# Kernel optimization log

Measured on AMD Instinct MI355X. Metric: run time of the kernel, lower is better.

## Reference

```python
import jax, jax.numpy as jnp
import numpy as np

T, H, NH, NKV, HD = 2048, 1024, 16, 4, 64
I, E, TOPK = 2048, 8, 2
EPS = 1e-5
ROPE_BASE = 10000.0


def rms_norm(x, w):
    var = jnp.mean(x * x, axis=-1, keepdims=True)
    return x * jax.lax.rsqrt(var + EPS) * w


def apply_rope(x, positions, n_heads):
    # neox-style rotary over full head_dim
    t = x.reshape(-1, n_heads, HD)
    half = HD // 2
    inv_freq = 1.0 / (ROPE_BASE ** (jnp.arange(0, half, dtype=jnp.float32) / half))
    freqs = positions.astype(jnp.float32)[:, None] * inv_freq[None, :]  # [T, half]
    cos = jnp.cos(freqs)[:, None, :]
    sin = jnp.sin(freqs)[:, None, :]
    x1, x2 = t[..., :half], t[..., half:]
    rot = jnp.concatenate([x1 * cos - x2 * sin, x2 * cos + x1 * sin], axis=-1)
    return rot.reshape(x.shape)


def setup_inputs():
    key = jax.random.key(0)
    ks = jax.random.split(key, 9)
    s = 0.02
    return dict(
        positions=jnp.arange(T, dtype=jnp.int32),
        hidden_states=jax.random.normal(ks[0], (T, H), jnp.float32),
        input_ln_w=jnp.ones((H,), jnp.float32),
        post_ln_w=jnp.ones((H,), jnp.float32),
        residual_ln_w=jnp.ones((H,), jnp.float32),
        qkv_w=jax.random.normal(ks[1], ((NH + 2 * NKV) * HD, H), jnp.float32) * s,
        o_w=jax.random.normal(ks[2], (H, NH * HD), jnp.float32) * s,
        gate_w=jax.random.normal(ks[3], (E, H), jnp.float32) * s,
        ws=jax.random.normal(ks[4], (E, 2 * I, H), jnp.float32) * s,
        w2s=jax.random.normal(ks[5], (E, H, I), jnp.float32) * s,
        res_w13=jax.random.normal(ks[6], (2 * H, H), jnp.float32) * s,
        res_w2=jax.random.normal(ks[7], (H, H), jnp.float32) * s,
    )


def attention(x, positions, qkv_w, o_w):
    qkv = x @ qkv_w.T  # [T, (NH+2*NKV)*HD]
    q, k, v = jnp.split(qkv, [NH * HD, NH * HD + NKV * HD], axis=-1)
    q = apply_rope(q, positions, NH)
    k = apply_rope(k, positions, NKV)
    q = q.reshape(T, NH, HD)
    k = k.reshape(T, NKV, HD)
    v = v.reshape(T, NKV, HD)
    rep = NH // NKV  # GQA: repeat kv heads
    k = jnp.repeat(k, rep, axis=1)
    v = jnp.repeat(v, rep, axis=1)
    scale = HD ** -0.5
    scores = jnp.einsum('tnd,snd->nts', q, k) * scale  # [NH, T, T]
    causal = jnp.tril(jnp.ones((T, T), dtype=bool))
    scores = jnp.where(causal[None], scores, -jnp.inf)
    probs = jax.nn.softmax(scores, axis=-1)
    out = jnp.einsum('nts,snd->tnd', probs, v).reshape(T, NH * HD)
    return out @ o_w.T


def silu_and_mul(gu):
    g, u = jnp.split(gu, 2, axis=-1)
    return jax.nn.silu(g) * u


def moe(x, gate_w, ws, w2s):
    logits = x @ gate_w.T  # [T, E]
    probs = jax.nn.softmax(logits, axis=-1)
    topk_w, topk_ids = jax.lax.top_k(probs, TOPK)
    topk_w = topk_w / jnp.sum(topk_w, axis=-1, keepdims=True)  # renormalize (top_k > 1)
    routes = jnp.zeros((x.shape[0], E), x.dtype).at[
        jnp.arange(x.shape[0])[:, None], topk_ids].set(topk_w)  # [T, E] sparse routing
    gu = jnp.einsum('th,eih->tei', x, ws)        # [T, E, 2I]
    act = silu_and_mul(gu)                        # [T, E, I]
    eo = jnp.einsum('tei,ehi->teh', act, w2s)     # [T, E, H]
    return jnp.einsum('te,teh->th', routes, eo)


def reference(positions, hidden_states, input_ln_w, post_ln_w, residual_ln_w,
              qkv_w, o_w, gate_w, ws, w2s, res_w13, res_w2):
    residual_input = hidden_states
    h = rms_norm(hidden_states, input_ln_w)
    h = attention(h, positions, qkv_w, o_w)
    residual_attn = residual_input + h
    # parallel residual MLP branch (ffn_dim == hidden)
    r = rms_norm(residual_attn, residual_ln_w)
    r = silu_and_mul(r @ res_w13.T) @ res_w2.T
    residual_mlp = residual_attn + r
    # MoE branch
    m = rms_norm(residual_attn, post_ln_w)
    m = moe(m, gate_w, ws, w2s)
    return residual_mlp + m
```

## Files before the change

kernel.cpp:

```cpp
#include <hip/hip_runtime.h>
#include <stdint.h>


typedef _Float16 f16;
typedef _Float16 f16x8 __attribute__((ext_vector_type(8)));
typedef _Float16 f16x4 __attribute__((ext_vector_type(4)));
typedef float f32x4 __attribute__((ext_vector_type(4)));

#define DEV __device__ __forceinline__

DEV void glds16(const void* g, void* l) {
  __builtin_amdgcn_global_load_lds((const __attribute__((address_space(1))) void*)g,
                                   (__attribute__((address_space(3))) void*)l, 16, 0, 0);
}

__global__ void cvt_f16_kernel(const float* __restrict__ in, f16* __restrict__ outp) {
  const size_t i = ((size_t)blockIdx.x * 256 + threadIdx.x) * 4;
  float4 f = *(const float4*)(in + i);
  f16x4 o;
  o[0] = (f16)f.x; o[1] = (f16)f.y; o[2] = (f16)f.z; o[3] = (f16)f.w;
  *(f16x4*)(outp + i) = o;
}

__global__ void cvt_f16x2_kernel(const float* __restrict__ in,
                                 f16* __restrict__ oh, f16* __restrict__ ol) {
  const size_t i = ((size_t)blockIdx.x * 256 + threadIdx.x) * 4;
  float4 f = *(const float4*)(in + i);
  f16x4 h, l;
  h[0] = (f16)f.x; l[0] = (f16)(f.x - (float)h[0]);
  h[1] = (f16)f.y; l[1] = (f16)(f.y - (float)h[1]);
  h[2] = (f16)f.z; l[2] = (f16)(f.z - (float)h[2]);
  h[3] = (f16)f.w; l[3] = (f16)(f.w - (float)h[3]);
  *(f16x4*)(oh + i) = h;
  *(f16x4*)(ol + i) = l;
}

__global__ void rmsnorm_kernel(const float* __restrict__ in, const float* __restrict__ w,
                               f16* __restrict__ outp) {
  const int t = blockIdx.x * 4 + (threadIdx.x >> 6);
  const int lane = threadIdx.x & 63;
  const float* x = in + (size_t)t * 1024;
  float v[16]; float ss = 0.f;
#pragma unroll
  for (int j = 0; j < 16; j++) { float a = x[lane + 64 * j]; v[j] = a; ss += a * a; }
#pragma unroll
  for (int m = 1; m < 64; m <<= 1) ss += __shfl_xor(ss, m);
  const float rs = rsqrtf(ss * (1.f / 1024.f) + 1e-5f);
#pragma unroll
  for (int j = 0; j < 16; j++)
    outp[(size_t)t * 1024 + lane + 64 * j] = (f16)(v[j] * rs * w[lane + 64 * j]);
}

__global__ void rmsnorm_dual_kernel(const float* __restrict__ in,
                                    const float* __restrict__ w1, const float* __restrict__ w2,
                                    f16* __restrict__ o1, f16* __restrict__ o2) {
  const int t = blockIdx.x * 4 + (threadIdx.x >> 6);
  const int lane = threadIdx.x & 63;
  const float* x = in + (size_t)t * 1024;
  float v[16]; float ss = 0.f;
#pragma unroll
  for (int j = 0; j < 16; j++) { float a = x[lane + 64 * j]; v[j] = a; ss += a * a; }
#pragma unroll
  for (int m = 1; m < 64; m <<= 1) ss += __shfl_xor(ss, m);
  const float rs = rsqrtf(ss * (1.f / 1024.f) + 1e-5f);
#pragma unroll
  for (int j = 0; j < 16; j++) {
    float nv = v[j] * rs;
    size_t idx = (size_t)t * 1024 + lane + 64 * j;
    o1[idx] = (f16)(nv * w1[lane + 64 * j]);
    o2[idx] = (f16)(nv * w2[lane + 64 * j]);
  }
}

template <int EPI, int BN>
__global__ __launch_bounds__(256) void gemm_f16_kernel(
    const f16* __restrict__ A, const f16* __restrict__ B,
    void* __restrict__ outp, const float* __restrict__ addsrc,
    int M, int N, int K) {
  constexpr int JT = BN / 32;
  __shared__ __attribute__((aligned(16))) f16 As[2][128 * 32];
  __shared__ __attribute__((aligned(16))) f16 Bs[2][BN * 32];
  const int tid = threadIdx.x;
  const size_t row0 = (size_t)blockIdx.y * 128, col0 = (size_t)blockIdx.x * BN;
  const int c0 = tid, c1 = tid + 256;
  const f16* a0 = A + (row0 + (c0 >> 2)) * K + (c0 & 3) * 8;
  const f16* a1 = A + (row0 + (c1 >> 2)) * K + (c1 & 3) * 8;
  const f16* b0 = B + (col0 + (c0 >> 2)) * K + (c0 & 3) * 8;
  const f16* b1 = B + (col0 + ((BN == 128) ? (c1 >> 2) : 0)) * K + (c1 & 3) * 8;

  const int wave = tid >> 6, lane = tid & 63, lr = lane >> 4, lc = lane & 15;
  const int wr = wave >> 1, wc = wave & 1;

  f32x4 acc[4][JT];
#pragma unroll
  for (int i = 0; i < 4; i++)
#pragma unroll
    for (int j = 0; j < JT; j++) acc[i][j] = (f32x4){0.f, 0.f, 0.f, 0.f};

  auto stage = [&](int k0, int buf) {
    glds16(a0 + k0, As[buf] + c0 * 8);
    glds16(a1 + k0, As[buf] + c1 * 8);
    glds16(b0 + k0, Bs[buf] + c0 * 8);
    if constexpr (BN == 128) glds16(b1 + k0, Bs[buf] + c1 * 8);
  };

  stage(0, 0);
  __syncthreads();
  int cur = 0;
  for (int k0 = 0; k0 < K; k0 += 32) {
    if (k0 + 32 < K) stage(k0 + 32, cur ^ 1);
    f16x8 af[4], bfr[JT];
#pragma unroll
    for (int i = 0; i < 4; i++)
      af[i] = *(const f16x8*)(As[cur] + (wr * 64 + i * 16 + lc) * 32 + lr * 8);
#pragma unroll
    for (int j = 0; j < JT; j++)
      bfr[j] = *(const f16x8*)(Bs[cur] + (wc * (BN / 2) + j * 16 + lc) * 32 + lr * 8);
#pragma unroll
    for (int i = 0; i < 4; i++)
#pragma unroll
      for (int j = 0; j < JT; j++)
        acc[i][j] = __builtin_amdgcn_mfma_f32_16x16x32_f16(af[i], bfr[j], acc[i][j], 0, 0, 0);
    __syncthreads();
    cur ^= 1;
  }

#pragma unroll
  for (int i = 0; i < 4; i++)
#pragma unroll
    for (int j = 0; j < JT; j++) {
      const size_t rbase = row0 + wr * 64 + i * 16 + lr * 4;
      const size_t col = col0 + wc * (BN / 2) + j * 16 + lc;
#pragma unroll
      for (int r = 0; r < 4; r++) {
        size_t idx = (rbase + r) * N + col;
        if constexpr (EPI == 0) ((float*)outp)[idx] = acc[i][j][r];
        else if constexpr (EPI == 1) ((float*)outp)[idx] = acc[i][j][r] + addsrc[idx];
        else ((f16*)outp)[idx] = (f16)acc[i][j][r];
      }
    }
}

__global__ __launch_bounds__(256) void gemm_f16x2_add_kernel(
    const f16* __restrict__ Ah, const f16* __restrict__ Al,
    const f16* __restrict__ Bh, const f16* __restrict__ Bl,
    float* __restrict__ outp, const float* __restrict__ addsrc,
    int M, int N, int K) {
  __shared__ __attribute__((aligned(16))) f16 Ash[2][128 * 32];
  __shared__ __attribute__((aligned(16))) f16 Asl[2][128 * 32];
  __shared__ __attribute__((aligned(16))) f16 Bsh[2][64 * 32];
  __shared__ __attribute__((aligned(16))) f16 Bsl[2][64 * 32];
  const int tid = threadIdx.x;
  const size_t row0 = (size_t)blockIdx.y * 128, col0 = (size_t)blockIdx.x * 64;
  const int c0 = tid, c1 = tid + 256;
  const size_t aoff0 = (row0 + (c0 >> 2)) * K + (c0 & 3) * 8;
  const size_t aoff1 = (row0 + (c1 >> 2)) * K + (c1 & 3) * 8;
  const size_t boff0 = (col0 + (c0 >> 2)) * K + (c0 & 3) * 8;

  const int wave = tid >> 6, lane = tid & 63, lr = lane >> 4, lc = lane & 15;
  const int wr = wave >> 1, wc = wave & 1;

  f32x4 acc[4][2];
#pragma unroll
  for (int i = 0; i < 4; i++)
#pragma unroll
    for (int j = 0; j < 2; j++) acc[i][j] = (f32x4){0.f, 0.f, 0.f, 0.f};

  auto stage = [&](int k0, int buf) {
    glds16(Ah + aoff0 + k0, Ash[buf] + c0 * 8);
    glds16(Ah + aoff1 + k0, Ash[buf] + c1 * 8);
    glds16(Al + aoff0 + k0, Asl[buf] + c0 * 8);
    glds16(Al + aoff1 + k0, Asl[buf] + c1 * 8);
    glds16(Bh + boff0 + k0, Bsh[buf] + c0 * 8);
    glds16(Bl + boff0 + k0, Bsl[buf] + c0 * 8);
  };

  stage(0, 0);
  __syncthreads();
  int cur = 0;
  for (int k0 = 0; k0 < K; k0 += 32) {
    if (k0 + 32 < K) stage(k0 + 32, cur ^ 1);
    f16x8 afh[4], afl[4], bfh[2], bfl[2];
#pragma unroll
    for (int i = 0; i < 4; i++) {
      const int ro = (wr * 64 + i * 16 + lc) * 32 + lr * 8;
      afh[i] = *(const f16x8*)(Ash[cur] + ro);
      afl[i] = *(const f16x8*)(Asl[cur] + ro);
    }
#pragma unroll
    for (int j = 0; j < 2; j++) {
      const int ro = (wc * 32 + j * 16 + lc) * 32 + lr * 8;
      bfh[j] = *(const f16x8*)(Bsh[cur] + ro);
      bfl[j] = *(const f16x8*)(Bsl[cur] + ro);
    }
#pragma unroll
    for (int i = 0; i < 4; i++)
#pragma unroll
      for (int j = 0; j < 2; j++) {
        acc[i][j] = __builtin_amdgcn_mfma_f32_16x16x32_f16(afh[i], bfh[j], acc[i][j], 0, 0, 0);
        acc[i][j] = __builtin_amdgcn_mfma_f32_16x16x32_f16(afh[i], bfl[j], acc[i][j], 0, 0, 0);
        acc[i][j] = __builtin_amdgcn_mfma_f32_16x16x32_f16(afl[i], bfh[j], acc[i][j], 0, 0, 0);
      }
    __syncthreads();
    cur ^= 1;
  }

#pragma unroll
  for (int i = 0; i < 4; i++)
#pragma unroll
    for (int j = 0; j < 2; j++) {
      const size_t rbase = row0 + wr * 64 + i * 16 + lr * 4;
      const size_t col = col0 + wc * 32 + j * 16 + lc;
#pragma unroll
      for (int r = 0; r < 4; r++) {
        size_t idx = (rbase + r) * N + col;
        outp[idx] = acc[i][j][r] + addsrc[idx];
      }
    }
}

template <int DIVROW, int BN>
__global__ __launch_bounds__(256) void gemm_moe_kernel(
    const f16* __restrict__ A, const f16* __restrict__ Ball, f16* __restrict__ outp,
    const int* __restrict__ perm, const int* __restrict__ counts,
    int N, int K, size_t strideB) {
  constexpr int JT = BN / 32;
  const int e = blockIdx.z;
  const int cnt = counts[e];
  const int bm = blockIdx.y;
  if (bm * 128 >= cnt) return;
  const f16* B = Ball + (size_t)e * strideB;
  __shared__ __attribute__((aligned(16))) f16 As[2][128 * 32];
  __shared__ __attribute__((aligned(16))) f16 Bs[2][BN * 32];
  const int tid = threadIdx.x;
  const size_t col0 = (size_t)blockIdx.x * BN;
  const int c0 = tid, c1 = tid + 256;
  const int pbase = e * 2048 + bm * 128;
  const int rt0 = c0 >> 2, rt1 = c1 >> 2;
  const int sid0 = (bm * 128 + rt0 < cnt) ? perm[pbase + rt0] : -1;
  const int sid1 = (bm * 128 + rt1 < cnt) ? perm[pbase + rt1] : -1;
  const size_t ar0 = DIVROW ? (size_t)(sid0 >> 1) : (size_t)sid0;
  const size_t ar1 = DIVROW ? (size_t)(sid1 >> 1) : (size_t)sid1;
  const f16* ap0 = A + ar0 * K + (c0 & 3) * 8;
  const f16* ap1 = A + ar1 * K + (c1 & 3) * 8;
  const f16* b0 = B + (col0 + (c0 >> 2)) * K + (c0 & 3) * 8;
  const f16* b1 = B + (col0 + ((BN == 128) ? (c1 >> 2) : 0)) * K + (c1 & 3) * 8;

  const int wave = tid >> 6, lane = tid & 63, lr = lane >> 4, lc = lane & 15;
  const int wr = wave >> 1, wc = wave & 1;

  f32x4 acc[4][JT];
#pragma unroll
  for (int i = 0; i < 4; i++)
#pragma unroll
    for (int j = 0; j < JT; j++) acc[i][j] = (f32x4){0.f, 0.f, 0.f, 0.f};

  auto stageB = [&](int k0, int buf) {
    glds16(b0 + k0, Bs[buf] + c0 * 8);
    if constexpr (BN == 128) glds16(b1 + k0, Bs[buf] + c1 * 8);
  };
  auto loadA = [&](int k0, f16x8& va0, f16x8& va1) {
#pragma unroll
    for (int x = 0; x < 8; x++) { va0[x] = (f16)0.f; va1[x] = (f16)0.f; }
    if (sid0 >= 0) va0 = *(const f16x8*)(ap0 + k0);
    if (sid1 >= 0) va1 = *(const f16x8*)(ap1 + k0);
  };

  f16x8 va0, va1;
  loadA(0, va0, va1);
  stageB(0, 0);
  *(f16x8*)(As[0] + c0 * 8) = va0;
  *(f16x8*)(As[0] + c1 * 8) = va1;
  __syncthreads();
  int cur = 0;
  for (int k0 = 0; k0 < K; k0 += 32) {
    const bool nxt = (k0 + 32 < K);
    if (nxt) { stageB(k0 + 32, cur ^ 1); loadA(k0 + 32, va0, va1); }
    f16x8 af[4], bfr[JT];
#pragma unroll
    for (int i = 0; i < 4; i++)
      af[i] = *(const f16x8*)(As[cur] + (wr * 64 + i * 16 + lc) * 32 + lr * 8);
#pragma unroll
    for (int j = 0; j < JT; j++)
      bfr[j] = *(const f16x8*)(Bs[cur] + (wc * (BN / 2) + j * 16 + lc) * 32 + lr * 8);
#pragma unroll
    for (int i = 0; i < 4; i++)
#pragma unroll
      for (int j = 0; j < JT; j++)
        acc[i][j] = __builtin_amdgcn_mfma_f32_16x16x32_f16(af[i], bfr[j], acc[i][j], 0, 0, 0);
    if (nxt) {
      *(f16x8*)(As[cur ^ 1] + c0 * 8) = va0;
      *(f16x8*)(As[cur ^ 1] + c1 * 8) = va1;
    }
    __syncthreads();
    cur ^= 1;
  }

  int sids[4][4];
#pragma unroll
  for (int i = 0; i < 4; i++)
#pragma unroll
    for (int r = 0; r < 4; r++) {
      int rit = wr * 64 + i * 16 + lr * 4 + r;
      sids[i][r] = (bm * 128 + rit < cnt) ? perm[pbase + rit] : -1;
    }
#pragma unroll
  for (int i = 0; i < 4; i++)
#pragma unroll
    for (int j = 0; j < JT; j++) {
      const size_t col = col0 + wc * (BN / 2) + j * 16 + lc;
#pragma unroll
      for (int r = 0; r < 4; r++)
        if (sids[i][r] >= 0)
          outp[(size_t)sids[i][r] * N + col] = (f16)acc[i][j][r];
    }
}

__global__ void rope_kernel(const float* __restrict__ qkv, const int* __restrict__ pos,
                            f16* __restrict__ qr, f16* __restrict__ kr) {
  const int t = blockIdx.y;
  const int u = blockIdx.x * 256 + threadIdx.x;
  if (u >= 640) return;
  const float* base = qkv + (size_t)t * 1536;
  const int head = u >> 5, i = u & 31;
  const bool isq = head < 16;
  const int off = isq ? head * 64 + i : 1024 + (head - 16) * 64 + i;
  const float x1 = base[off], x2 = base[off + 32];
  const double ph = (double)pos[t] * exp((double)i * -0.28782313662425575);
  const float c = (float)cos(ph), s = (float)sin(ph);
  const float r1 = x1 * c - x2 * s, r2 = x2 * c + x1 * s;
  if (isq) {
    const float qs = 0.18033688011116042f;
    qr[(size_t)t * 1024 + head * 64 + i] = (f16)(qs * r1);
    qr[(size_t)t * 1024 + head * 64 + i + 32] = (f16)(qs * r2);
  } else {
    const int kh = head - 16;
    kr[(size_t)t * 256 + kh * 64 + i] = (f16)r1;
    kr[(size_t)t * 256 + kh * 64 + i + 32] = (f16)r2;
  }
}

__global__ void vtrans_kernel(const float* __restrict__ qkvf, f16* __restrict__ vt) {
  __shared__ float Ts[64 * 69];
  const int t0 = blockIdx.x * 64;
  const int kv = blockIdx.y;
  const int tid = threadIdx.x;
  const int tr = tid >> 2, jj = tid & 3;
  const float* src = qkvf + (size_t)(t0 + tr) * 1536 + 1280 + kv * 64 + jj * 16;
#pragma unroll
  for (int x = 0; x < 4; x++) {
    float4 f = *(const float4*)(src + x * 4);
    Ts[tr * 69 + jj * 16 + x * 4 + 0] = f.x;
    Ts[tr * 69 + jj * 16 + x * 4 + 1] = f.y;
    Ts[tr * 69 + jj * 16 + x * 4 + 2] = f.z;
    Ts[tr * 69 + jj * 16 + x * 4 + 3] = f.w;
  }
  __syncthreads();
  f16* dst = vt + (size_t)(kv * 64 + tr) * 2048 + t0 + jj * 16;
#pragma unroll
  for (int x = 0; x < 2; x++) {
    f16x8 o;
#pragma unroll
    for (int i = 0; i < 8; i++) o[i] = (f16)Ts[(jj * 16 + x * 8 + i) * 69 + tr];
    *(f16x8*)(dst + x * 8) = o;
  }
}

__global__ __launch_bounds__(256, 3) void attn_kernel(
    const f16* __restrict__ qr, const f16* __restrict__ kr, const f16* __restrict__ vt,
    f16* __restrict__ ahi, f16* __restrict__ alo) {
  const int qt = 31 - (int)blockIdx.x;
  const int h = blockIdx.y;
  const int kvh = h >> 2;
  __shared__ __attribute__((aligned(16))) f16 Ks[128 * 72];
  __shared__ __attribute__((aligned(16))) f16 Vs[64 * 136];
  __shared__ __attribute__((aligned(16))) f16 Pl[4 * 16 * 136];
  const int tid = threadIdx.x;
  const int wave = tid >> 6, lane = tid & 63, lr = lane >> 4, lc = lane & 15;
  const int trow = qt * 64 + wave * 16 + lc;
  f16* Pw = Pl + wave * 16 * 136;

  const int krow = tid >> 3, kcol = (tid & 7) * 8;
  const int vrow = tid >> 4, vcol = (tid & 15) * 8;
  const f16* kgbase = kr + (size_t)kvh * 64 + kcol;
  const f16* vgbase = vt + (size_t)(kvh * 64 + vrow) * 2048 + vcol;

  const f16* qp = qr + (size_t)trow * 1024 + h * 64 + lr * 8;
  f16x8 qf0 = *(const f16x8*)(qp);
  f16x8 qf1 = *(const f16x8*)(qp + 32);

  float m_run = -3e38f, l_run = 0.f;
  f32x4 accO[4];
#pragma unroll
  for (int jo = 0; jo < 4; jo++) accO[jo] = (f32x4){0.f, 0.f, 0.f, 0.f};

  const int nch = (qt >> 1) + 1;

  f16x8 kreg[4], vreg[4];
#pragma unroll
  for (int it = 0; it < 4; it++) {
    kreg[it] = *(const f16x8*)(kgbase + (size_t)(it * 32 + krow) * 256);
    vreg[it] = *(const f16x8*)(vgbase + it * 16 * 2048);
  }

  for (int ch = 0; ch < nch; ++ch) {
    const int c0 = ch * 128;
    const bool last = (ch == nch - 1);

    __syncthreads();
#pragma unroll
    for (int it = 0; it < 4; it++) {
      *(f16x8*)(Ks + (it * 32 + krow) * 72 + kcol) = kreg[it];
      *(f16x8*)(Vs + (it * 16 + vrow) * 136 + vcol) = vreg[it];
    }
    __syncthreads();

    if (!last) {
      const int c1 = c0 + 128;
#pragma unroll
      for (int it = 0; it < 4; it++) {
        kreg[it] = *(const f16x8*)(kgbase + (size_t)(c1 + it * 32 + krow) * 256);
        vreg[it] = *(const f16x8*)(vgbase + it * 16 * 2048 + c1);
      }
    }

    f32x4 st[8];
#pragma unroll
    for (int j = 0; j < 8; j++) {
      const f16* kp = Ks + (j * 16 + lc) * 72 + lr * 8;
      f16x8 ka0 = *(const f16x8*)(kp);
      f16x8 ka1 = *(const f16x8*)(kp + 32);
      f32x4 s = (f32x4){0.f, 0.f, 0.f, 0.f};
      s = __builtin_amdgcn_mfma_f32_16x16x32_f16(ka0, qf0, s, 0, 0, 0);
      s = __builtin_amdgcn_mfma_f32_16x16x32_f16(ka1, qf1, s, 0, 0, 0);
      st[j] = s;
    }

    if (last) {
#pragma unroll
      for (int j = 0; j < 8; j++)
#pragma unroll
        for (int r = 0; r < 4; r++)
          if (c0 + j * 16 + lr * 4 + r > trow) st[j][r] = -3e38f;
    }

    float mc = -3e38f;
#pragma unroll
    for (int j = 0; j < 8; j++)
      mc = fmaxf(mc, fmaxf(fmaxf(st[j][0], st[j][1]), fmaxf(st[j][2], st[j][3])));
    mc = fmaxf(mc, __shfl_xor(mc, 16));
    mc = fmaxf(mc, __shfl_xor(mc, 32));
    const float mn = fmaxf(m_run, mc);
    const float alpha = __builtin_amdgcn_exp2f(m_run - mn);
    m_run = mn;

    float ls = 0.f;
#pragma unroll
    for (int j = 0; j < 8; j++) {
      f16x4 pv;
#pragma unroll
      for (int r = 0; r < 4; r++) {
        float e = __builtin_amdgcn_exp2f(st[j][r] - mn);
        ls += e;
        pv[r] = (f16)e;
      }
      *(f16x4*)(Pw + lc * 136 + j * 16 + lr * 4) = pv;
    }
    ls += __shfl_xor(ls, 16);
    ls += __shfl_xor(ls, 32);
    l_run = l_run * alpha + ls;
#pragma unroll
    for (int jo = 0; jo < 4; jo++) accO[jo] *= alpha;

#pragma unroll
    for (int kkt = 0; kkt < 4; kkt++) {
      f16x8 pb = *(const f16x8*)(Pw + lc * 136 + kkt * 32 + lr * 8);
#pragma unroll
      for (int jo = 0; jo < 4; jo++) {
        f16x8 va = *(const f16x8*)(Vs + (jo * 16 + lc) * 136 + kkt * 32 + lr * 8);
        accO[jo] = __builtin_amdgcn_mfma_f32_16x16x32_f16(va, pb, accO[jo], 0, 0, 0);
      }
    }
  }

  const float inv = 1.f / l_run;
#pragma unroll
  for (int jo = 0; jo < 4; jo++) {
    f16x4 hi4, lo4;
#pragma unroll
    for (int r = 0; r < 4; r++) {
      float o = accO[jo][r] * inv;
      f16 hv = (f16)o;
      hi4[r] = hv;
      lo4[r] = (f16)(o - (float)hv);
    }
    const size_t idx = (size_t)trow * 1024 + h * 64 + jo * 16 + lr * 4;
    *(f16x4*)(ahi + idx) = hi4;
    *(f16x4*)(alo + idx) = lo4;
  }
}

__global__ void routing_kernel(const float* __restrict__ resA,
                               const float* __restrict__ postw,
                               const float* __restrict__ gw,
                               int* __restrict__ counts, int* __restrict__ perm,
                               float* __restrict__ rw) {
  const int t = blockIdx.x * 4 + (threadIdx.x >> 6);
  const int lane = threadIdx.x & 63;
  const float* x = resA + (size_t)t * 1024;
  float v[16]; float ss = 0.f;
#pragma unroll
  for (int j = 0; j < 16; j++) { float a = x[lane + 64 * j]; v[j] = a; ss += a * a; }
#pragma unroll
  for (int m = 1; m < 64; m <<= 1) ss += __shfl_xor(ss, m);
  const float rs = rsqrtf(ss * (1.f / 1024.f) + 1e-5f);
#pragma unroll
  for (int j = 0; j < 16; j++) v[j] *= rs * postw[lane + 64 * j];
  float lg[8];
#pragma unroll
  for (int e = 0; e < 8; e++) {
    float p = 0.f;
    const float* g = gw + (size_t)e * 1024;
#pragma unroll
    for (int j = 0; j < 16; j++) p += v[j] * g[lane + 64 * j];
#pragma unroll
    for (int m = 1; m < 64; m <<= 1) p += __shfl_xor(p, m);
    lg[e] = p;
  }
  if (lane == 0) {
    int e0 = 0; float b0 = lg[0];
#pragma unroll
    for (int e = 1; e < 8; e++) if (lg[e] > b0) { b0 = lg[e]; e0 = e; }
    int e1 = -1; float b1 = -3e38f;
#pragma unroll
    for (int e = 0; e < 8; e++) if (e != e0 && lg[e] > b1) { b1 = lg[e]; e1 = e; }
    const float w0 = 1.f / (1.f + expf(b1 - b0));
    const float w1 = 1.f - w0;
    int p0 = atomicAdd(&counts[e0], 1);
    perm[e0 * 2048 + p0] = t * 2;
    int p1 = atomicAdd(&counts[e1], 1);
    perm[e1 * 2048 + p1] = t * 2 + 1;
    rw[t * 2] = w0;
    rw[t * 2 + 1] = w1;
  }
}

__global__ void silu_mul_kernel(const f16* __restrict__ gu, f16* __restrict__ outp, int lgN) {
  const int N = 1 << lgN;
  const size_t i4 = ((size_t)blockIdx.x * 256 + threadIdx.x) * 4;
  const size_t r = i4 >> lgN;
  const int c = (int)(i4 & (N - 1));
  const f16* gp = gu + r * (size_t)(2 * N) + c;
  f16x4 g = *(const f16x4*)gp;
  f16x4 u = *(const f16x4*)(gp + N);
  f16x4 o;
#pragma unroll
  for (int x = 0; x < 4; x++) {
    float gg = (float)g[x], uu = (float)u[x];
    o[x] = (f16)(gg / (1.f + __expf(-gg)) * uu);
  }
  *(f16x4*)(outp + r * (size_t)N + c) = o;
}

__global__ void final_add_kernel(float* __restrict__ outp, const f16* __restrict__ eo,
                                 const float* __restrict__ rw) {
  const size_t i4 = ((size_t)blockIdx.x * 256 + threadIdx.x) * 4;
  const int t = (int)(i4 >> 10);
  const int c = (int)(i4 & 1023);
  const float w0 = rw[2 * t], w1 = rw[2 * t + 1];
  f16x4 a = *(const f16x4*)(eo + ((size_t)(2 * t)) * 1024 + c);
  f16x4 b = *(const f16x4*)(eo + ((size_t)(2 * t + 1)) * 1024 + c);
  float4 o = *(float4*)(outp + i4);
  o.x += w0 * (float)a[0] + w1 * (float)b[0];
  o.y += w0 * (float)a[1] + w1 * (float)b[1];
  o.z += w0 * (float)a[2] + w1 * (float)b[2];
  o.w += w0 * (float)a[3] + w1 * (float)b[3];
  *(float4*)(outp + i4) = o;
}

extern "C" void kernel_launch(void* const* d_in, const int* in_sizes, int n_in,
                              void* d_out, int out_size, void* d_ws, size_t ws_size,
                              hipStream_t stream) {
  const int* positions = (const int*)d_in[0];
  const float* hidden = (const float*)d_in[1];
  const float* in_ln = (const float*)d_in[2];
  const float* post_ln = (const float*)d_in[3];
  const float* res_ln = (const float*)d_in[4];
  const float* qkv_w = (const float*)d_in[5];
  const float* o_w = (const float*)d_in[6];
  const float* gate_w = (const float*)d_in[7];
  const float* ws_w = (const float*)d_in[8];
  const float* w2s_w = (const float*)d_in[9];
  const float* w13_w = (const float*)d_in[10];
  const float* w2_w = (const float*)d_in[11];
  float* out = (float*)d_out;

  char* p = (char*)d_ws;
  auto alloc = [&](size_t b) { void* r = (void*)p; p += (b + 255) & ~(size_t)255; return r; };

  f16* wqkv = (f16*)alloc((size_t)1536 * 1024 * 2);
  f16* woh  = (f16*)alloc((size_t)1024 * 1024 * 2);
  f16* wol  = (f16*)alloc((size_t)1024 * 1024 * 2);
  f16* wws  = (f16*)alloc((size_t)8 * 4096 * 1024 * 2);
  f16* ww2  = (f16*)alloc((size_t)8 * 1024 * 2048 * 2);
  f16* w13  = (f16*)alloc((size_t)2048 * 1024 * 2);
  f16* w2c  = (f16*)alloc((size_t)1024 * 1024 * 2);
  f16* hn   = (f16*)alloc((size_t)2048 * 1024 * 2);
  float* qkvf = (float*)alloc((size_t)2048 * 1536 * 4);
  f16* qr = (f16*)alloc((size_t)2048 * 1024 * 2);
  f16* kr = (f16*)alloc((size_t)2048 * 256 * 2);
  f16* vt = (f16*)alloc((size_t)256 * 2048 * 2);
  f16* ath = (f16*)alloc((size_t)2048 * 1024 * 2);
  f16* atl = (f16*)alloc((size_t)2048 * 1024 * 2);
  float* resA = (float*)alloc((size_t)2048 * 1024 * 4);
  f16* rn = (f16*)alloc((size_t)2048 * 1024 * 2);
  f16* mn = (f16*)alloc((size_t)2048 * 1024 * 2);
  f16* gu13 = (f16*)alloc((size_t)2048 * 2048 * 2);
  f16* act13 = (f16*)alloc((size_t)2048 * 1024 * 2);
  f16* gum = (f16*)alloc((size_t)4096 * 4096 * 2);
  f16* actm = (f16*)alloc((size_t)4096 * 2048 * 2);
  f16* eo = (f16*)alloc((size_t)4096 * 1024 * 2);
  float* rw = (float*)alloc((size_t)4096 * 4);
  int* counts = (int*)alloc(256);
  int* perm = (int*)alloc((size_t)8 * 2048 * 4);

  cvt_f16_kernel<<<dim3(1536 * 1024 / 1024), dim3(256), 0, stream>>>(qkv_w, wqkv);
  cvt_f16_kernel<<<dim3(8 * 4096 * 1024 / 1024), dim3(256), 0, stream>>>(ws_w, wws);
  cvt_f16_kernel<<<dim3(8 * 1024 * 2048 / 1024), dim3(256), 0, stream>>>(w2s_w, ww2);
  cvt_f16_kernel<<<dim3(2048 * 1024 / 1024), dim3(256), 0, stream>>>(w13_w, w13);
  cvt_f16_kernel<<<dim3(1024 * 1024 / 1024), dim3(256), 0, stream>>>(w2_w, w2c);
  cvt_f16x2_kernel<<<dim3(1024 * 1024 / 1024), dim3(256), 0, stream>>>(o_w, woh, wol);
  hipMemsetAsync(counts, 0, 256, stream);

  rmsnorm_kernel<<<dim3(512), dim3(256), 0, stream>>>(hidden, in_ln, hn);
  gemm_f16_kernel<0, 64><<<dim3(24, 16), dim3(256), 0, stream>>>(
      hn, wqkv, (void*)qkvf, (const float*)nullptr, 2048, 1536, 1024);
  rope_kernel<<<dim3(3, 2048), dim3(256), 0, stream>>>(qkvf, positions, qr, kr);
  vtrans_kernel<<<dim3(32, 4), dim3(256), 0, stream>>>(qkvf, vt);
  attn_kernel<<<dim3(32, 16), dim3(256), 0, stream>>>(qr, kr, vt, ath, atl);
  gemm_f16x2_add_kernel<<<dim3(16, 16), dim3(256), 0, stream>>>(
      ath, atl, woh, wol, resA, hidden, 2048, 1024, 1024);

  rmsnorm_dual_kernel<<<dim3(512), dim3(256), 0, stream>>>(resA, res_ln, post_ln, rn, mn);
  routing_kernel<<<dim3(512), dim3(256), 0, stream>>>(resA, post_ln, gate_w, counts, perm, rw);

  gemm_f16_kernel<2, 64><<<dim3(32, 16), dim3(256), 0, stream>>>(
      rn, w13, (void*)gu13, (const float*)nullptr, 2048, 2048, 1024);
  silu_mul_kernel<<<dim3(2048 * 1024 / 1024), dim3(256), 0, stream>>>(gu13, act13, 10);
  gemm_f16_kernel<1, 64><<<dim3(16, 16), dim3(256), 0, stream>>>(
      act13, w2c, (void*)out, resA, 2048, 1024, 1024);

  gemm_moe_kernel<1, 128><<<dim3(32, 16, 8), dim3(256), 0, stream>>>(
      mn, wws, gum, perm, counts, 4096, 1024, (size_t)4096 * 1024);
  silu_mul_kernel<<<dim3(4096 * 2048 / 1024), dim3(256), 0, stream>>>(gum, actm, 11);
  gemm_moe_kernel<0, 128><<<dim3(8, 16, 8), dim3(256), 0, stream>>>(
      actm, ww2, eo, perm, counts, 1024, 2048, (size_t)1024 * 2048);
  final_add_kernel<<<dim3(2048 * 1024 / 1024), dim3(256), 0, stream>>>(out, eo, rw);
}
```

Before: 661.1 us.

## Split-K the small GEMMs and MoE down projection, reducing partials in consumers

Adds a split-K template parameter to the dense, f16x2 and MoE GEMM kernels. The QKV, O-proj, residual down-proj and MoE down-proj GEMMs now write fp32 partial results, which are summed by rope/vtrans, a new add3 kernel, or final_add4. The goal is more blocks and better CU occupancy for GEMMs whose grids are small (256 to 384 blocks). The cost is extra fp32 partial-buffer traffic, two extra elementwise launches, and fp32 instead of f16 expert outputs, which is a 4x split for the MoE output.

After: 642.8 us. 1.03x faster.

```diff
diff --git a/kernel.cpp b/kernel.cpp
--- a/kernel.cpp
+++ b/kernel.cpp
@@ -72,7 +72,7 @@
   }
 }
 
-template <int EPI, int BN>
+template <int EPI, int BN, int SPLITK = 1>
 __global__ __launch_bounds__(256) void gemm_f16_kernel(
     const f16* __restrict__ A, const f16* __restrict__ B,
     void* __restrict__ outp, const float* __restrict__ addsrc,
@@ -82,6 +82,8 @@
   __shared__ __attribute__((aligned(16))) f16 Bs[2][BN * 32];
   const int tid = threadIdx.x;
   const size_t row0 = (size_t)blockIdx.y * 128, col0 = (size_t)blockIdx.x * BN;
+  const int ks = (SPLITK > 1) ? (int)blockIdx.z : 0;
+  const int kspan = K / SPLITK, kb = ks * kspan;
   const int c0 = tid, c1 = tid + 256;
   const f16* a0 = A + (row0 + (c0 >> 2)) * K + (c0 & 3) * 8;
   const f16* a1 = A + (row0 + (c1 >> 2)) * K + (c1 & 3) * 8;
@@ -104,11 +106,11 @@
     if constexpr (BN == 128) glds16(b1 + k0, Bs[buf] + c1 * 8);
   };
 
-  stage(0, 0);
+  stage(kb, 0);
   __syncthreads();
   int cur = 0;
-  for (int k0 = 0; k0 < K; k0 += 32) {
-    if (k0 + 32 < K) stage(k0 + 32, cur ^ 1);
+  for (int k0 = kb; k0 < kb + kspan; k0 += 32) {
+    if (k0 + 32 < kb + kspan) stage(k0 + 32, cur ^ 1);
     f16x8 af[4], bfr[JT];
 #pragma unroll
     for (int i = 0; i < 4; i++)
@@ -134,13 +136,16 @@
 #pragma unroll
       for (int r = 0; r < 4; r++) {
         size_t idx = (rbase + r) * N + col;
-        if constexpr (EPI == 0) ((float*)outp)[idx] = acc[i][j][r];
+        if constexpr (SPLITK > 1) {
+          ((float*)outp)[(size_t)ks * M * N + idx] = acc[i][j][r];
+        } else if constexpr (EPI == 0) ((float*)outp)[idx] = acc[i][j][r];
         else if constexpr (EPI == 1) ((float*)outp)[idx] = acc[i][j][r] + addsrc[idx];
         else ((f16*)outp)[idx] = (f16)acc[i][j][r];
       }
     }
 }
 
+template <int SPLITK>
 __global__ __launch_bounds__(256) void gemm_f16x2_add_kernel(
     const f16* __restrict__ Ah, const f16* __restrict__ Al,
     const f16* __restrict__ Bh, const f16* __restrict__ Bl,
@@ -152,6 +157,8 @@
   __shared__ __attribute__((aligned(16))) f16 Bsl[2][64 * 32];
   const int tid = threadIdx.x;
   const size_t row0 = (size_t)blockIdx.y * 128, col0 = (size_t)blockIdx.x * 64;
+  const int ks = (SPLITK > 1) ? (int)blockIdx.z : 0;
+  const int kspan = K / SPLITK, kb = ks * kspan;
   const int c0 = tid, c1 = tid + 256;
   const size_t aoff0 = (row0 + (c0 >> 2)) * K + (c0 & 3) * 8;
   const size_t aoff1 = (row0 + (c1 >> 2)) * K + (c1 & 3) * 8;
@@ -175,11 +182,11 @@
     glds16(Bl + boff0 + k0, Bsl[buf] + c0 * 8);
   };
 
-  stage(0, 0);
+  stage(kb, 0);
   __syncthreads();
   int cur = 0;
-  for (int k0 = 0; k0 < K; k0 += 32) {
-    if (k0 + 32 < K) stage(k0 + 32, cur ^ 1);
+  for (int k0 = kb; k0 < kb + kspan; k0 += 32) {
+    if (k0 + 32 < kb + kspan) stage(k0 + 32, cur ^ 1);
     f16x8 afh[4], afl[4], bfh[2], bfl[2];
 #pragma unroll
     for (int i = 0; i < 4; i++) {
@@ -214,21 +221,24 @@
 #pragma unroll
       for (int r = 0; r < 4; r++) {
         size_t idx = (rbase + r) * N + col;
-        outp[idx] = acc[i][j][r] + addsrc[idx];
+        if constexpr (SPLITK > 1) outp[(size_t)ks * M * N + idx] = acc[i][j][r];
+        else outp[idx] = acc[i][j][r] + addsrc[idx];
       }
     }
 }
 
-template <int DIVROW, int BN>
+template <int DIVROW, int BN, int SPLITK = 1>
 __global__ __launch_bounds__(256) void gemm_moe_kernel(
-    const f16* __restrict__ A, const f16* __restrict__ Ball, f16* __restrict__ outp,
+    const f16* __restrict__ A, const f16* __restrict__ Ball, void* __restrict__ outp,
     const int* __restrict__ perm, const int* __restrict__ counts,
     int N, int K, size_t strideB) {
   constexpr int JT = BN / 32;
-  const int e = blockIdx.z;
+  const int e = (int)blockIdx.z / SPLITK;
+  const int ks = (int)blockIdx.z % SPLITK;
   const int cnt = counts[e];
   const int bm = blockIdx.y;
   if (bm * 128 >= cnt) return;
+  const int kspan = K / SPLITK, kb = ks * kspan;
   const f16* B = Ball + (size_t)e * strideB;
   __shared__ __attribute__((aligned(16))) f16 As[2][128 * 32];
   __shared__ __attribute__((aligned(16))) f16 Bs[2][BN * 32];
@@ -267,14 +277,14 @@
   };
 
   f16x8 va0, va1;
-  loadA(0, va0, va1);
-  stageB(0, 0);
+  loadA(kb, va0, va1);
+  stageB(kb, 0);
   *(f16x8*)(As[0] + c0 * 8) = va0;
   *(f16x8*)(As[0] + c1 * 8) = va1;
   __syncthreads();
   int cur = 0;
-  for (int k0 = 0; k0 < K; k0 += 32) {
-    const bool nxt = (k0 + 32 < K);
+  for (int k0 = kb; k0 < kb + kspan; k0 += 32) {
+    const bool nxt = (k0 + 32 < kb + kspan);
     if (nxt) { stageB(k0 + 32, cur ^ 1); loadA(k0 + 32, va0, va1); }
     f16x8 af[4], bfr[JT];
 #pragma unroll
@@ -311,8 +321,12 @@
       const size_t col = col0 + wc * (BN / 2) + j * 16 + lc;
 #pragma unroll
       for (int r = 0; r < 4; r++)
-        if (sids[i][r] >= 0)
-          outp[(size_t)sids[i][r] * N + col] = (f16)acc[i][j][r];
+        if (sids[i][r] >= 0) {
+          if constexpr (SPLITK > 1)
+            ((float*)outp)[((size_t)ks * 4096 + sids[i][r]) * N + col] = acc[i][j][r];
+          else
+            ((f16*)outp)[(size_t)sids[i][r] * N + col] = (f16)acc[i][j][r];
+        }
     }
 }
 
@@ -321,11 +335,12 @@
   const int t = blockIdx.y;
   const int u = blockIdx.x * 256 + threadIdx.x;
   if (u >= 640) return;
-  const float* base = qkv + (size_t)t * 1536;
+  const float* b0 = qkv + (size_t)t * 1536;
+  const float* b1 = b0 + (size_t)2048 * 1536;
   const int head = u >> 5, i = u & 31;
   const bool isq = head < 16;
   const int off = isq ? head * 64 + i : 1024 + (head - 16) * 64 + i;
-  const float x1 = base[off], x2 = base[off + 32];
+  const float x1 = b0[off] + b1[off], x2 = b0[off + 32] + b1[off + 32];
   const double ph = (double)pos[t] * exp((double)i * -0.28782313662425575);
   const float c = (float)cos(ph), s = (float)sin(ph);
   const float r1 = x1 * c - x2 * s, r2 = x2 * c + x1 * s;
@@ -346,14 +361,16 @@
   const int kv = blockIdx.y;
   const int tid = threadIdx.x;
   const int tr = tid >> 2, jj = tid & 3;
-  const float* src = qkvf + (size_t)(t0 + tr) * 1536 + 1280 + kv * 64 + jj * 16;
+  const float* src0 = qkvf + (size_t)(t0 + tr) * 1536 + 1280 + kv * 64 + jj * 16;
+  const float* src1 = src0 + (size_t)2048 * 1536;
 #pragma unroll
   for (int x = 0; x < 4; x++) {
-    float4 f = *(const float4*)(src + x * 4);
-    Ts[tr * 69 + jj * 16 + x * 4 + 0] = f.x;
-    Ts[tr * 69 + jj * 16 + x * 4 + 1] = f.y;
-    Ts[tr * 69 + jj * 16 + x * 4 + 2] = f.z;
-    Ts[tr * 69 + jj * 16 + x * 4 + 3] = f.w;
+    float4 f = *(const float4*)(src0 + x * 4);
+    float4 g = *(const float4*)(src1 + x * 4);
+    Ts[tr * 69 + jj * 16 + x * 4 + 0] = f.x + g.x;
+    Ts[tr * 69 + jj * 16 + x * 4 + 1] = f.y + g.y;
+    Ts[tr * 69 + jj * 16 + x * 4 + 2] = f.z + g.z;
+    Ts[tr * 69 + jj * 16 + x * 4 + 3] = f.w + g.w;
   }
   __syncthreads();
   f16* dst = vt + (size_t)(kv * 64 + tr) * 2048 + t0 + jj * 16;
@@ -364,6 +381,19 @@
     for (int i = 0; i < 8; i++) o[i] = (f16)Ts[(jj * 16 + x * 8 + i) * 69 + tr];
     *(f16x8*)(dst + x * 8) = o;
   }
+}
+
+__global__ void add3_kernel(float* __restrict__ o, const float* __restrict__ a,
+                            const float* __restrict__ p0, const float* __restrict__ p1) {
+  const size_t i4 = ((size_t)blockIdx.x * 256 + threadIdx.x) * 4;
+  float4 va = *(const float4*)(a + i4);
+  float4 v0 = *(const float4*)(p0 + i4);
+  float4 v1 = *(const float4*)(p1 + i4);
+  va.x += v0.x + v1.x;
+  va.y += v0.y + v1.y;
+  va.z += v0.z + v1.z;
+  va.w += v0.w + v1.w;
+  *(float4*)(o + i4) = va;
 }
 
 __global__ __launch_bounds__(256, 3) void attn_kernel(
@@ -562,19 +592,26 @@
   *(f16x4*)(outp + r * (size_t)N + c) = o;
 }
 
-__global__ void final_add_kernel(float* __restrict__ outp, const f16* __restrict__ eo,
-                                 const float* __restrict__ rw) {
+__global__ void final_add4_kernel(float* __restrict__ outp, const float* __restrict__ eo4,
+                                  const float* __restrict__ rw) {
   const size_t i4 = ((size_t)blockIdx.x * 256 + threadIdx.x) * 4;
   const int t = (int)(i4 >> 10);
   const int c = (int)(i4 & 1023);
   const float w0 = rw[2 * t], w1 = rw[2 * t + 1];
-  f16x4 a = *(const f16x4*)(eo + ((size_t)(2 * t)) * 1024 + c);
-  f16x4 b = *(const f16x4*)(eo + ((size_t)(2 * t + 1)) * 1024 + c);
+  float4 s0 = {0.f, 0.f, 0.f, 0.f}, s1 = {0.f, 0.f, 0.f, 0.f};
+#pragma unroll
+  for (int ks = 0; ks < 4; ks++) {
+    const float* p = eo4 + (size_t)ks * 4096 * 1024;
+    float4 a = *(const float4*)(p + (size_t)(2 * t) * 1024 + c);
+    float4 b = *(const float4*)(p + (size_t)(2 * t + 1) * 1024 + c);
+    s0.x += a.x; s0.y += a.y; s0.z += a.z; s0.w += a.w;
+    s1.x += b.x; s1.y += b.y; s1.z += b.z; s1.w += b.w;
+  }
   float4 o = *(float4*)(outp + i4);
-  o.x += w0 * (float)a[0] + w1 * (float)b[0];
-  o.y += w0 * (float)a[1] + w1 * (float)b[1];
-  o.z += w0 * (float)a[2] + w1 * (float)b[2];
-  o.w += w0 * (float)a[3] + w1 * (float)b[3];
+  o.x += w0 * s0.x + w1 * s1.x;
+  o.y += w0 * s0.y + w1 * s1.y;
+  o.z += w0 * s0.z + w1 * s1.z;
+  o.w += w0 * s0.w + w1 * s1.w;
   *(float4*)(outp + i4) = o;
 }
 
@@ -606,20 +643,22 @@
   f16* w13  = (f16*)alloc((size_t)2048 * 1024 * 2);
   f16* w2c  = (f16*)alloc((size_t)1024 * 1024 * 2);
   f16* hn   = (f16*)alloc((size_t)2048 * 1024 * 2);
-  float* qkvf = (float*)alloc((size_t)2048 * 1536 * 4);
+  float* qkvp = (float*)alloc((size_t)2 * 2048 * 1536 * 4);
   f16* qr = (f16*)alloc((size_t)2048 * 1024 * 2);
   f16* kr = (f16*)alloc((size_t)2048 * 256 * 2);
   f16* vt = (f16*)alloc((size_t)256 * 2048 * 2);
   f16* ath = (f16*)alloc((size_t)2048 * 1024 * 2);
   f16* atl = (f16*)alloc((size_t)2048 * 1024 * 2);
+  float* opp = (float*)alloc((size_t)2 * 2048 * 1024 * 4);
   float* resA = (float*)alloc((size_t)2048 * 1024 * 4);
   f16* rn = (f16*)alloc((size_t)2048 * 1024 * 2);
   f16* mn = (f16*)alloc((size_t)2048 * 1024 * 2);
   f16* gu13 = (f16*)alloc((size_t)2048 * 2048 * 2);
   f16* act13 = (f16*)alloc((size_t)2048 * 1024 * 2);
+  float* w2p = (float*)alloc((size_t)2 * 2048 * 1024 * 4);
   f16* gum = (f16*)alloc((size_t)4096 * 4096 * 2);
   f16* actm = (f16*)alloc((size_t)4096 * 2048 * 2);
-  f16* eo = (f16*)alloc((size_t)4096 * 1024 * 2);
+  float* eo4 = (float*)alloc((size_t)4 * 4096 * 1024 * 4);
   float* rw = (float*)alloc((size_t)4096 * 4);
   int* counts = (int*)alloc(256);
   int* perm = (int*)alloc((size_t)8 * 2048 * 4);
@@ -633,13 +672,15 @@
   hipMemsetAsync(counts, 0, 256, stream);
 
   rmsnorm_kernel<<<dim3(512), dim3(256), 0, stream>>>(hidden, in_ln, hn);
-  gemm_f16_kernel<0, 64><<<dim3(24, 16), dim3(256), 0, stream>>>(
-      hn, wqkv, (void*)qkvf, (const float*)nullptr, 2048, 1536, 1024);
-  rope_kernel<<<dim3(3, 2048), dim3(256), 0, stream>>>(qkvf, positions, qr, kr);
-  vtrans_kernel<<<dim3(32, 4), dim3(256), 0, stream>>>(qkvf, vt);
+  gemm_f16_kernel<0, 64, 2><<<dim3(24, 16, 2), dim3(256), 0, stream>>>(
+      hn, wqkv, (void*)qkvp, (const float*)nullptr, 2048, 1536, 1024);
+  rope_kernel<<<dim3(3, 2048), dim3(256), 0, stream>>>(qkvp, positions, qr, kr);
+  vtrans_kernel<<<dim3(32, 4), dim3(256), 0, stream>>>(qkvp, vt);
   attn_kernel<<<dim3(32, 16), dim3(256), 0, stream>>>(qr, kr, vt, ath, atl);
-  gemm_f16x2_add_kernel<<<dim3(16, 16), dim3(256), 0, stream>>>(
-      ath, atl, woh, wol, resA, hidden, 2048, 1024, 1024);
+  gemm_f16x2_add_kernel<2><<<dim3(16, 16, 2), dim3(256), 0, stream>>>(
+      ath, atl, woh, wol, opp, (const float*)nullptr, 2048, 1024, 1024);
+  add3_kernel<<<dim3(2048), dim3(256), 0, stream>>>(
+      resA, hidden, opp, opp + (size_t)2048 * 1024);
 
   rmsnorm_dual_kernel<<<dim3(512), dim3(256), 0, stream>>>(resA, res_ln, post_ln, rn, mn);
   routing_kernel<<<dim3(512), dim3(256), 0, stream>>>(resA, post_ln, gate_w, counts, perm, rw);
@@ -647,13 +688,15 @@
   gemm_f16_kernel<2, 64><<<dim3(32, 16), dim3(256), 0, stream>>>(
       rn, w13, (void*)gu13, (const float*)nullptr, 2048, 2048, 1024);
   silu_mul_kernel<<<dim3(2048 * 1024 / 1024), dim3(256), 0, stream>>>(gu13, act13, 10);
-  gemm_f16_kernel<1, 64><<<dim3(16, 16), dim3(256), 0, stream>>>(
-      act13, w2c, (void*)out, resA, 2048, 1024, 1024);
+  gemm_f16_kernel<0, 64, 2><<<dim3(16, 16, 2), dim3(256), 0, stream>>>(
+      act13, w2c, (void*)w2p, (const float*)nullptr, 2048, 1024, 1024);
+  add3_kernel<<<dim3(2048), dim3(256), 0, stream>>>(
+      out, resA, w2p, w2p + (size_t)2048 * 1024);
 
   gemm_moe_kernel<1, 128><<<dim3(32, 16, 8), dim3(256), 0, stream>>>(
-      mn, wws, gum, perm, counts, 4096, 1024, (size_t)4096 * 1024);
+      mn, wws, (void*)gum, perm, counts, 4096, 1024, (size_t)4096 * 1024);
   silu_mul_kernel<<<dim3(4096 * 2048 / 1024), dim3(256), 0, stream>>>(gum, actm, 11);
-  gemm_moe_kernel<0, 128><<<dim3(8, 16, 8), dim3(256), 0, stream>>>(
-      actm, ww2, eo, perm, counts, 1024, 2048, (size_t)1024 * 2048);
-  final_add_kernel<<<dim3(2048 * 1024 / 1024), dim3(256), 0, stream>>>(out, eo, rw);
-}
+  gemm_moe_kernel<0, 128, 4><<<dim3(8, 16, 32), dim3(256), 0, stream>>>(
+      actm, ww2, (void*)eo4, perm, counts, 1024, 2048, (size_t)1024 * 2048);
+  final_add4_kernel<<<dim3(2048 * 1024 / 1024), dim3(256), 0, stream>>>(out, eo4, rw);
+}
```
